# Kernel optimization log

Measured on AMD Instinct MI355X. Metric: run time of the kernel, lower is better.

The kernel has to match this reference:

```python
import jax, jax.numpy as jnp
import numpy as np

K = 16
ITERS = 5
DIST_CHUNK = 8  # feature-chunk size to avoid materializing [B,F,S,S]


def pairwise_l1(x):
    """x: [B, F, S] -> d: [B, S, S], d[b,i,j] = ||x[b,:,i]-x[b,:,j]||_1.
    Computed in feature chunks via scan so peak intermediate is [B,CH,S,S]."""
    B, F, S = x.shape
    xc = x.reshape(B, F // DIST_CHUNK, DIST_CHUNK, S).transpose(1, 0, 2, 3)  # [F/CH,B,CH,S]

    def step(acc, blk):  # blk: [B, CH, S]
        return acc + jnp.abs(blk[:, :, :, None] - blk[:, :, None, :]).sum(axis=1), None

    d, _ = jax.lax.scan(step, jnp.zeros((B, S, S), x.dtype), xc)
    return d


def kmedoids_pool(x, w):
    B, F, S = x.shape
    wm = jnp.mean(w, axis=1)                       # [B,S] per-token attention weight
    d = pairwise_l1(x)                             # [B,S,S]
    _, ctr = jax.lax.top_k(wm, K)                  # [B,K] initial medoids
    dw = d * wm[:, None, :]                        # d[b,i,j]*w[b,j]
    for _ in range(ITERS):
        # distance from every token to each current medoid: [B,S,K]
        i2c = jnp.take_along_axis(d, jnp.broadcast_to(ctr[:, None, :], (B, S, K)), axis=2)
        assign = jnp.argmin(i2c, axis=2)           # [B,S] cluster assignment
        member = jax.nn.one_hot(assign, K, dtype=x.dtype)  # [B,S,K]
        # weighted within-cluster cost for candidate i in cluster k:
        # cost[b,i,k] = sum_j d[b,i,j]*w[b,j]*member[b,j,k]
        cost = jnp.einsum('bij,bjk->bik', dw, member)
        cost = jnp.where(member > 0, cost, jnp.inf)  # medoid must be a member
        ctr = jnp.argmin(cost, axis=1)             # [B,K] new medoids
    idx = jnp.broadcast_to(ctr[:, None, :], (B, F, K))
    return jnp.take_along_axis(x, idx, axis=2)     # [B,F,K]


def setup_inputs() -> dict:
    key = jax.random.key(0)
    kx, kw = jax.random.split(key)
    B, F, S = 8, 256, 1024
    x = jax.random.normal(kx, (B, F, S), dtype=jnp.float32)
    w = jax.random.uniform(kw, (B, S, S), dtype=jnp.float32)
    return {"x": x, "w": w}


def reference(x, w):
    return kmedoids_pool(x, w)
```

## Files before the change

### kernel.cpp

```cpp
#include <hip/hip_runtime.h>
#include <math.h>

#define BB 8
#define FF 256
#define SS 1024
#define KK 16
#define ITERS 5

typedef unsigned long long ull;


#define ICH 8
__global__ void wm_part_kernel(const float* __restrict__ w, float* __restrict__ part) {
    int j = blockIdx.x * 256 + threadIdx.x;
    int ic = blockIdx.y, b = blockIdx.z;
    const float* wp = w + (size_t)b * SS * SS + (size_t)ic * (SS / ICH) * SS + j;
    float s = 0.f;
#pragma unroll 16
    for (int i = 0; i < SS / ICH; ++i) s += wp[(size_t)i * SS];
    part[((size_t)ic * BB + b) * SS + j] = s;
}

#define FCD 8
#define TS 64
#define NT (SS / TS)
__device__ __forceinline__ void async_copy16(const float* g, const float* s) {
    __builtin_amdgcn_global_load_lds((const __attribute__((address_space(1))) void*)g,
                                     (__attribute__((address_space(3))) void*)s, 16, 0, 0);
}

__global__ __launch_bounds__(128, 4) void dist_kernel(const float* __restrict__ x,
                                                      float* __restrict__ d) {
    __shared__ float smem[2048];
    int tid = threadIdx.x;
    int wave = tid >> 6, lane = tid & 63;
    int b = blockIdx.y;
    int w = blockIdx.x;
    int it = 0, rem = w;
    while (rem >= NT - it) { rem -= NT - it; ++it; }
    int jt = it + rem;
    int i0 = it * TS, j0 = jt * TS;
    const float* xb = x + (size_t)b * FF * SS;
    float* db = d + (size_t)b * SS * SS;
    int rl = wave * 32 + (lane >> 3) * 4;
    int cl = (lane & 7) * 8;
    int sF = tid >> 4, sT = (tid & 15) * 4;

    float acc[4][8] = {};

    auto stage = [&](int c, int h) {
        float* A = smem + h * 1024 + wave * 256;
        const float* base = xb + ((size_t)c * FCD + sF) * SS + sT;
        async_copy16(base + i0, A);
        async_copy16(base + j0, A + 512);
    };
    auto compute = [&](int h) {
        const float* A = smem + h * 1024;
        const float* B = A + 512;
#pragma unroll
        for (int f = 0; f < FCD; ++f) {
            float4 a4 = *(const float4*)(A + f * 64 + rl);
            float4 b0 = *(const float4*)(B + f * 64 + cl);
            float4 b1 = *(const float4*)(B + f * 64 + cl + 4);
            float av[4] = {a4.x, a4.y, a4.z, a4.w};
            float bv[8] = {b0.x, b0.y, b0.z, b0.w, b1.x, b1.y, b1.z, b1.w};
#pragma unroll
            for (int r = 0; r < 4; ++r)
#pragma unroll
                for (int c = 0; c < 8; ++c)
                    acc[r][c] += fabsf(av[r] - bv[c]);
        }
    };

    stage(0, 0);
#pragma unroll 1
    for (int k = 0; k < FF / FCD - 1; ++k) {
        asm volatile("s_barrier" ::: "memory");
        stage(k + 1, (k + 1) & 1);
        asm volatile("s_waitcnt vmcnt(2)" ::: "memory");
        asm volatile("s_barrier" ::: "memory");
        compute(k & 1);
    }
    asm volatile("s_waitcnt vmcnt(0)" ::: "memory");
    asm volatile("s_barrier" ::: "memory");
    compute(1);

#pragma unroll
    for (int r = 0; r < 4; ++r) {
        float4 v0 = make_float4(acc[r][0], acc[r][1], acc[r][2], acc[r][3]);
        float4 v1 = make_float4(acc[r][4], acc[r][5], acc[r][6], acc[r][7]);
        float* row = &db[(size_t)(i0 + rl + r) * SS + j0 + cl];
        *(float4*)row = v0;
        *(float4*)(row + 4) = v1;
    }
    if (it != jt) {
#pragma unroll
        for (int c = 0; c < 8; ++c) {
            float4 v = make_float4(acc[0][c], acc[1][c], acc[2][c], acc[3][c]);
            *(float4*)&db[(size_t)(j0 + cl + c) * SS + i0 + rl] = v;
        }
    }
}

__global__ __launch_bounds__(1024) void topk_assign_kernel(const float* __restrict__ part,
                                                           float* __restrict__ wm,
                                                           const float* __restrict__ d,
                                                           int* __restrict__ assign) {
    int b = blockIdx.x;
    int tid = threadIdx.x;
    int lane = tid & 63, wv = tid >> 6;
    __shared__ ull red[16];
    __shared__ int ctr_s[KK];
    float v = 0.f;
#pragma unroll
    for (int ic = 0; ic < ICH; ++ic) v += part[((size_t)ic * BB + b) * SS + tid];
    v *= (1.0f / SS);
    wm[b * SS + tid] = v;
    ull key = (((ull)__float_as_uint(v)) << 32) | (ull)(0xFFFFFFFFu - (unsigned)tid);
    for (int k = 0; k < KK; ++k) {
        ull kk = key;
#pragma unroll
        for (int off = 32; off; off >>= 1) {
            ull o = __shfl_down(kk, off, 64);
            if (o > kk) kk = o;
        }
        if (lane == 0) red[wv] = kk;
        __syncthreads();
        if (wv == 0) {
            ull k2 = (lane < 16) ? red[lane] : 0ull;
#pragma unroll
            for (int off = 8; off; off >>= 1) {
                ull o = __shfl_down(k2, off, 64);
                if (o > k2) k2 = o;
            }
            if (lane == 0) red[0] = k2;
        }
        __syncthreads();
        ull W = red[0];
        int widx = (int)(0xFFFFFFFFu - (unsigned)(W & 0xFFFFFFFFu));
        if (tid == widx) key = 0;
        if (tid == 0) ctr_s[k] = widx;
        __syncthreads();
    }
    const float* db = d + (size_t)b * SS * SS;
    float bv = INFINITY;
    int bk = 0;
#pragma unroll
    for (int k = 0; k < KK; ++k) {
        float vv = db[(size_t)ctr_s[k] * SS + tid];
        if (vv < bv) { bv = vv; bk = k; }
    }
    assign[b * SS + tid] = bk;
}

#define RPB 16
__global__ __launch_bounds__(256) void cost_kernel(const float* __restrict__ d,
                                                   const float* __restrict__ wm,
                                                   const int* __restrict__ assign,
                                                   float* __restrict__ cost) {
    int b = blockIdx.y;
    int tid = threadIdx.x;
    int lane = tid & 63, wv = tid >> 6;
    __shared__ float wmv[SS];
    __shared__ int asg[SS];
    *(float4*)&wmv[tid * 4] = *(const float4*)&wm[b * SS + tid * 4];
    *(int4*)&asg[tid * 4] = *(const int4*)&assign[b * SS + tid * 4];
    __syncthreads();
    const float* db = d + (size_t)b * SS * SS;
#pragma unroll
    for (int r = 0; r < RPB / 4; ++r) {
        int i = blockIdx.x * RPB + wv * (RPB / 4) + r;
        int my = asg[i];
        const float* drow = db + (size_t)i * SS;
        float s = 0.f;
#pragma unroll
        for (int c = 0; c < SS / 256; ++c) {
            int j = c * 256 + lane * 4;
            float4 dv = *(const float4*)&drow[j];
            float4 wv4 = *(const float4*)&wmv[j];
            int4 a4 = *(const int4*)&asg[j];
            s += (a4.x == my) ? dv.x * wv4.x : 0.f;
            s += (a4.y == my) ? dv.y * wv4.y : 0.f;
            s += (a4.z == my) ? dv.z * wv4.z : 0.f;
            s += (a4.w == my) ? dv.w * wv4.w : 0.f;
        }
#pragma unroll
        for (int off = 32; off; off >>= 1) s += __shfl_down(s, off, 64);
        if (lane == 0) cost[b * SS + i] = s;
    }
}

__global__ __launch_bounds__(1024) void update_assign_kernel(
        const float* __restrict__ d, const float* __restrict__ cost,
        int* __restrict__ assign, const float* __restrict__ x,
        float* __restrict__ out, int last) {
    int b = blockIdx.y;
    int q = blockIdx.x;
    int tid = threadIdx.x;
    int lane = tid & 63, wv = tid >> 6;
    __shared__ float cost_s[SS];
    __shared__ int assign_s[SS];
    __shared__ int ctr_s[KK];
    __shared__ ull pk[4][256];
    cost_s[tid] = cost[b * SS + tid];
    assign_s[tid] = assign[b * SS + tid];
    __syncthreads();
    ull best = ~0ull;
    int k = wv;
    for (int c = 0; c < SS / 64; ++c) {
        int i = c * 64 + lane;
        if (assign_s[i] == k) {
            ull key = (((ull)__float_as_uint(cost_s[i])) << 32) | (unsigned)i;
            if (key < best) best = key;
        }
    }
#pragma unroll
    for (int off = 32; off; off >>= 1) {
        ull o = __shfl_down(best, off, 64);
        if (o < best) best = o;
    }
    if (lane == 0) ctr_s[k] = (best == ~0ull) ? 0 : (int)(best & 0xFFFFFFFFu);
    __syncthreads();
    const float* db = d + (size_t)b * SS * SS;
    if (!last) {
        int tok = q * 256 + (tid & 255);
        int g = tid >> 8;
        ull bk = ~0ull;
#pragma unroll
        for (int kk = 0; kk < 4; ++kk) {
            int k2 = g * 4 + kk;
            float vv = db[(size_t)ctr_s[k2] * SS + tok];
            ull key = (((ull)__float_as_uint(vv)) << 32) | (unsigned)k2;
            if (key < bk) bk = key;
        }
        pk[g][tid & 255] = bk;
        __syncthreads();
        if (tid < 256) {
            ull m = pk[0][tid];
            if (pk[1][tid] < m) m = pk[1][tid];
            if (pk[2][tid] < m) m = pk[2][tid];
            if (pk[3][tid] < m) m = pk[3][tid];
            assign[b * SS + q * 256 + tid] = (int)(m & 0xFFFFFFFFu);
        }
    } else {
        int e = q * 1024 + tid;
        int f = e / KK, k2 = e % KK;
        out[((size_t)b * FF + f) * KK + k2] = x[((size_t)b * FF + f) * SS + ctr_s[k2]];
    }
}

extern "C" void kernel_launch(void* const* d_in, const int* in_sizes, int n_in,
                              void* d_out, int out_size, void* d_ws, size_t ws_size,
                              hipStream_t stream) {
    const float* x = (const float*)d_in[0];
    const float* w = (const float*)d_in[1];
    float* out = (float*)d_out;

    char* ws = (char*)d_ws;
    float* d = (float*)ws;
    size_t off = (size_t)BB * SS * SS * sizeof(float);
    float* wm = (float*)(ws + off);   off += (size_t)BB * SS * sizeof(float);
    int* assign = (int*)(ws + off);   off += (size_t)BB * SS * sizeof(int);
    float* cost = (float*)(ws + off); off += (size_t)BB * SS * sizeof(float);
    float* part = (float*)(ws + off);

    dist_kernel<<<dim3(136, BB), 128, 0, stream>>>(x, d);
    wm_part_kernel<<<dim3(SS / 256, ICH, BB), 256, 0, stream>>>(w, part);
    topk_assign_kernel<<<BB, 1024, 0, stream>>>(part, wm, d, assign);
    for (int itr = 0; itr < ITERS; ++itr) {
        cost_kernel<<<dim3(SS / RPB, BB), 256, 0, stream>>>(d, wm, assign, cost);
        update_assign_kernel<<<dim3(4, BB), 1024, 0, stream>>>(d, cost, assign, x, out,
                                                               itr == ITERS - 1 ? 1 : 0);
    }
}
```

Measured before the change: 252.6 us.

## Deepen dist_kernel LDS pipeline and fuse cost/update via last-block counter

The distance kernel moves from a double buffer to a six-slot LDS ring with four chunks prefetched, processing two feature chunks per barrier pair, so global-load latency is better hidden. The cost and update_assign kernels are merged: each cost block bumps a per-batch atomic counter, and the last block to finish picks medoids and recomputes assignments or writes the output. This halves the per-iteration launch count and removes a launch gap, but the final serial step now runs on one 256-thread block per batch instead of four 1024-thread blocks. Counters reuse the 'part' buffer after topk_assign has consumed it, cleared with a memset.

```diff
diff --git a/kernel.cpp b/kernel.cpp
--- a/kernel.cpp
+++ b/kernel.cpp
@@ -31,7 +31,7 @@
 
 __global__ __launch_bounds__(128, 4) void dist_kernel(const float* __restrict__ x,
                                                       float* __restrict__ d) {
-    __shared__ float smem[2048];
+    __shared__ float smem[6 * 1024];
     int tid = threadIdx.x;
     int wave = tid >> 6, lane = tid & 63;
     int b = blockIdx.y;
@@ -48,14 +48,14 @@
 
     float acc[4][8] = {};
 
-    auto stage = [&](int c, int h) {
-        float* A = smem + h * 1024 + wave * 256;
+    auto stage = [&](int c) {
+        float* A = smem + (c % 6) * 1024 + wave * 256;
         const float* base = xb + ((size_t)c * FCD + sF) * SS + sT;
         async_copy16(base + i0, A);
         async_copy16(base + j0, A + 512);
     };
-    auto compute = [&](int h) {
-        const float* A = smem + h * 1024;
+    auto compute = [&](int c) {
+        const float* A = smem + (c % 6) * 1024;
         const float* B = A + 512;
 #pragma unroll
         for (int f = 0; f < FCD; ++f) {
@@ -67,23 +67,26 @@
 #pragma unroll
             for (int r = 0; r < 4; ++r)
 #pragma unroll
-                for (int c = 0; c < 8; ++c)
-                    acc[r][c] += fabsf(av[r] - bv[c]);
+                for (int c2 = 0; c2 < 8; ++c2)
+                    acc[r][c2] += fabsf(av[r] - bv[c2]);
         }
     };
 
-    stage(0, 0);
+    stage(0); stage(1); stage(2); stage(3);
 #pragma unroll 1
-    for (int k = 0; k < FF / FCD - 1; ++k) {
+    for (int p = 0; p < FF / FCD; p += 2) {
         asm volatile("s_barrier" ::: "memory");
-        stage(k + 1, (k + 1) & 1);
-        asm volatile("s_waitcnt vmcnt(2)" ::: "memory");
+        if (p < 28) {
+            stage(p + 4); stage(p + 5);
+            asm volatile("s_waitcnt vmcnt(8)" ::: "memory");
+        } else if (p == 28) {
+            asm volatile("s_waitcnt vmcnt(4)" ::: "memory");
+        } else {
+            asm volatile("s_waitcnt vmcnt(0)" ::: "memory");
+        }
         asm volatile("s_barrier" ::: "memory");
-        compute(k & 1);
-    }
-    asm volatile("s_waitcnt vmcnt(0)" ::: "memory");
-    asm volatile("s_barrier" ::: "memory");
-    compute(1);
+        compute(p); compute(p + 1);
+    }
 
 #pragma unroll
     for (int r = 0; r < 4; ++r) {
@@ -154,22 +157,27 @@
 }
 
 #define RPB 16
-__global__ __launch_bounds__(256) void cost_kernel(const float* __restrict__ d,
-                                                   const float* __restrict__ wm,
-                                                   const int* __restrict__ assign,
-                                                   float* __restrict__ cost) {
+__global__ __launch_bounds__(256) void cost_update_kernel(
+        const float* __restrict__ d, const float* __restrict__ wm,
+        int* __restrict__ assign, float* __restrict__ cost,
+        const float* __restrict__ x, float* __restrict__ out,
+        int* __restrict__ counter, int last) {
     int b = blockIdx.y;
+    int ib = blockIdx.x;
     int tid = threadIdx.x;
     int lane = tid & 63, wv = tid >> 6;
     __shared__ float wmv[SS];
     __shared__ int asg[SS];
+    __shared__ float cost_s[SS];
+    __shared__ int ctr_s[KK];
+    __shared__ int lastflag;
     *(float4*)&wmv[tid * 4] = *(const float4*)&wm[b * SS + tid * 4];
     *(int4*)&asg[tid * 4] = *(const int4*)&assign[b * SS + tid * 4];
     __syncthreads();
     const float* db = d + (size_t)b * SS * SS;
 #pragma unroll
     for (int r = 0; r < RPB / 4; ++r) {
-        int i = blockIdx.x * RPB + wv * (RPB / 4) + r;
+        int i = ib * RPB + wv * (RPB / 4) + r;
         int my = asg[i];
         const float* drow = db + (size_t)i * SS;
         float s = 0.f;
@@ -188,64 +196,50 @@
         for (int off = 32; off; off >>= 1) s += __shfl_down(s, off, 64);
         if (lane == 0) cost[b * SS + i] = s;
     }
-}
-
-__global__ __launch_bounds__(1024) void update_assign_kernel(
-        const float* __restrict__ d, const float* __restrict__ cost,
-        int* __restrict__ assign, const float* __restrict__ x,
-        float* __restrict__ out, int last) {
-    int b = blockIdx.y;
-    int q = blockIdx.x;
-    int tid = threadIdx.x;
-    int lane = tid & 63, wv = tid >> 6;
-    __shared__ float cost_s[SS];
-    __shared__ int assign_s[SS];
-    __shared__ int ctr_s[KK];
-    __shared__ ull pk[4][256];
-    cost_s[tid] = cost[b * SS + tid];
-    assign_s[tid] = assign[b * SS + tid];
-    __syncthreads();
-    ull best = ~0ull;
-    int k = wv;
-    for (int c = 0; c < SS / 64; ++c) {
-        int i = c * 64 + lane;
-        if (assign_s[i] == k) {
-            ull key = (((ull)__float_as_uint(cost_s[i])) << 32) | (unsigned)i;
-            if (key < best) best = key;
-        }
-    }
-#pragma unroll
-    for (int off = 32; off; off >>= 1) {
-        ull o = __shfl_down(best, off, 64);
-        if (o < best) best = o;
-    }
-    if (lane == 0) ctr_s[k] = (best == ~0ull) ? 0 : (int)(best & 0xFFFFFFFFu);
-    __syncthreads();
-    const float* db = d + (size_t)b * SS * SS;
+    __threadfence();
+    if (tid == 0) lastflag = (atomicAdd(&counter[b], 1) == (int)gridDim.x - 1);
+    __syncthreads();
+    if (!lastflag) return;
+    __threadfence();
+    *(float4*)&cost_s[tid * 4] = *(const float4*)&cost[b * SS + tid * 4];
+    __syncthreads();
+#pragma unroll
+    for (int q = 0; q < 4; ++q) {
+        int k = wv + q * 4;
+        ull best = ~0ull;
+        for (int c = 0; c < SS / 64; ++c) {
+            int i = c * 64 + lane;
+            if (asg[i] == k) {
+                ull key = (((ull)__float_as_uint(cost_s[i])) << 32) | (unsigned)i;
+                if (key < best) best = key;
+            }
+        }
+#pragma unroll
+        for (int off = 32; off; off >>= 1) {
+            ull o = __shfl_down(best, off, 64);
+            if (o < best) best = o;
+        }
+        if (lane == 0) ctr_s[k] = (best == ~0ull) ? 0 : (int)(best & 0xFFFFFFFFu);
+    }
+    __syncthreads();
     if (!last) {
-        int tok = q * 256 + (tid & 255);
-        int g = tid >> 8;
-        ull bk = ~0ull;
-#pragma unroll
-        for (int kk = 0; kk < 4; ++kk) {
-            int k2 = g * 4 + kk;
-            float vv = db[(size_t)ctr_s[k2] * SS + tok];
-            ull key = (((ull)__float_as_uint(vv)) << 32) | (unsigned)k2;
-            if (key < bk) bk = key;
-        }
-        pk[g][tid & 255] = bk;
-        __syncthreads();
-        if (tid < 256) {
-            ull m = pk[0][tid];
-            if (pk[1][tid] < m) m = pk[1][tid];
-            if (pk[2][tid] < m) m = pk[2][tid];
-            if (pk[3][tid] < m) m = pk[3][tid];
-            assign[b * SS + q * 256 + tid] = (int)(m & 0xFFFFFFFFu);
+#pragma unroll
+        for (int q = 0; q < 4; ++q) {
+            int tok = q * 256 + tid;
+            ull bk = ~0ull;
+#pragma unroll
+            for (int k = 0; k < KK; ++k) {
+                float vv = db[(size_t)ctr_s[k] * SS + tok];
+                ull key = (((ull)__float_as_uint(vv)) << 32) | (unsigned)k;
+                if (key < bk) bk = key;
+            }
+            assign[b * SS + tok] = (int)(bk & 0xFFFFFFFFu);
         }
     } else {
-        int e = q * 1024 + tid;
-        int f = e / KK, k2 = e % KK;
-        out[((size_t)b * FF + f) * KK + k2] = x[((size_t)b * FF + f) * SS + ctr_s[k2]];
+        for (int e = tid; e < FF * KK; e += 256) {
+            int f = e / KK, k2 = e % KK;
+            out[((size_t)b * FF + f) * KK + k2] = x[((size_t)b * FF + f) * SS + ctr_s[k2]];
+        }
     }
 }
 
@@ -263,13 +257,15 @@
     int* assign = (int*)(ws + off);   off += (size_t)BB * SS * sizeof(int);
     float* cost = (float*)(ws + off); off += (size_t)BB * SS * sizeof(float);
     float* part = (float*)(ws + off);
+    int* counters = (int*)part;
 
     dist_kernel<<<dim3(136, BB), 128, 0, stream>>>(x, d);
     wm_part_kernel<<<dim3(SS / 256, ICH, BB), 256, 0, stream>>>(w, part);
     topk_assign_kernel<<<BB, 1024, 0, stream>>>(part, wm, d, assign);
+    hipMemsetAsync(counters, 0, ITERS * BB * sizeof(int), stream);
     for (int itr = 0; itr < ITERS; ++itr) {
-        cost_kernel<<<dim3(SS / RPB, BB), 256, 0, stream>>>(d, wm, assign, cost);
-        update_assign_kernel<<<dim3(4, BB), 1024, 0, stream>>>(d, cost, assign, x, out,
-                                                               itr == ITERS - 1 ? 1 : 0);
-    }
-}
+        cost_update_kernel<<<dim3(SS / RPB, BB), 256, 0, stream>>>(
+            d, wm, assign, cost, x, out, counters + itr * BB,
+            itr == ITERS - 1 ? 1 : 0);
+    }
+}
```

After: 482.4 us. +91.0%, slower.
